# Optimization experiments

Hardware: AMD Instinct MI355X
Metric: run time of the kernel (lower is better)

Reference implementation:

```python
import jax, jax.numpy as jnp
import numpy as np

N_NODES = 50000
N_EDGES = 800000
D_IN, H1, H2, N_CLASSES = 128, 128, 64, 2


def setup_inputs() -> dict:
    key = jax.random.key(0)
    ks = jax.random.split(key, 8)
    x = jax.random.normal(ks[0], (N_NODES, D_IN), dtype=jnp.float32)
    edge_index = jax.random.randint(ks[1], (2, N_EDGES), 0, N_NODES, dtype=jnp.int64)
    s = 1.0 / np.sqrt(D_IN)
    W1 = jax.random.uniform(ks[2], (D_IN, H1), jnp.float32, -s, s)
    b1 = jnp.zeros((H1,), jnp.float32)
    s = 1.0 / np.sqrt(H1)
    W2 = jax.random.uniform(ks[3], (H1, H2), jnp.float32, -s, s)
    b2 = jnp.zeros((H2,), jnp.float32)
    s = 1.0 / np.sqrt(H2)
    Wo = jax.random.uniform(ks[4], (H2, N_CLASSES), jnp.float32, -s, s)
    bo = jax.random.uniform(ks[5], (N_CLASSES,), jnp.float32, -s, s)
    return {"x": x, "edge_index": edge_index, "W1": W1, "b1": b1,
            "W2": W2, "b2": b2, "Wo": Wo, "bo": bo}


def _gcn_conv(x, W, b, src, dst, n_nodes):
    # PyG GCNConv: add self loops, symmetric normalization deg^{-1/2} A deg^{-1/2}
    h = x @ W  # [N, out]
    ones = jnp.ones((src.shape[0],), h.dtype)
    deg = jax.ops.segment_sum(ones, dst, num_segments=n_nodes) + 1.0  # +1 self loop
    dinv = jax.lax.rsqrt(deg)  # deg >= 1 always (self loops)
    coef = dinv[src] * dinv[dst]  # [E]
    msg = h[src] * coef[:, None]  # [E, out] gather
    agg = jax.ops.segment_sum(msg, dst, num_segments=n_nodes)  # scatter-add
    agg = agg + h * (dinv * dinv)[:, None]  # self-loop contribution
    return agg + b


def reference(x, edge_index, W1, b1, W2, b2, Wo, bo):
    src, dst = edge_index[0], edge_index[1]
    n = x.shape[0]
    h = jax.nn.relu(_gcn_conv(x, W1, b1, src, dst, n))
    # dropout p=0.25 is identity in eval mode
    h = jax.nn.relu(_gcn_conv(h, W2, b2, src, dst, n))
    logits = h @ Wo + bo
    return jax.nn.log_softmax(logits, axis=1)
```

## Files before the change

kernel.cpp:

```cpp
#include <hip/hip_runtime.h>
#include <stdint.h>

#define N_NODES 50000
#define N_EDGES 800000
#define CAP 80
#define ZROW N_NODES
#define SCAT_BLOCKS 391
#define GEMM_BLOCKS 782
#define CNT(v) ((v) << 4)

typedef __attribute__((ext_vector_type(8))) short short8;
typedef __attribute__((ext_vector_type(4))) float floatx4;

__device__ __forceinline__ float bflo(uint32_t u) { return __uint_as_float(u << 16); }
__device__ __forceinline__ float bfhi(uint32_t u) { return __uint_as_float(u & 0xffff0000u); }
__device__ __forceinline__ unsigned short f2b(float f) {
    uint32_t u = __float_as_uint(f);
    u += 0x7fffu + ((u >> 16) & 1u);
    return (unsigned short)(u >> 16);
}

__global__ void k_prep(const float* __restrict__ W1, const float* __restrict__ W2,
                       unsigned short* __restrict__ Wt1, unsigned short* __restrict__ Wt2,
                       int* __restrict__ counts) {
    int gid = blockIdx.x * 256 + threadIdx.x;
    if (gid < 16384) {
        int k = gid >> 7, n = gid & 127;
        Wt1[n * 128 + k] = f2b(W1[gid]);
    } else if (gid < 24576) {
        int j = gid - 16384;
        int k = j >> 6, n = j & 63;
        Wt2[n * 128 + k] = f2b(W2[j]);
    } else if (gid < 24576 + 802816) {
        counts[gid - 24576] = 0;
    }
}

__global__ __launch_bounds__(256) void k_scat_gemm1(const int* __restrict__ src,
                                                    const int* __restrict__ dst,
                                                    int* __restrict__ counts,
                                                    int* __restrict__ csr,
                                                    const float* __restrict__ x,
                                                    const unsigned short* __restrict__ Wt1,
                                                    unsigned short* __restrict__ h1s,
                                                    unsigned short* __restrict__ h2s) {
    __shared__ unsigned short At[64 * 136];
    __shared__ unsigned short Bt[128 * 136];
    int t = threadIdx.x;
    if (blockIdx.x < SCAT_BLOCKS) {
        int i = blockIdx.x * 256 + t;
        if (i >= N_EDGES / 8) return;
        const int4* s4 = (const int4*)(src + i * 8);
        const int4* d4 = (const int4*)(dst + i * 8);
        int4 sa = s4[0], sb = s4[1];
        int4 da = d4[0], db = d4[1];
        int r0 = atomicAdd(&counts[CNT(da.x)], 1);
        int r1 = atomicAdd(&counts[CNT(da.y)], 1);
        int r2 = atomicAdd(&counts[CNT(da.z)], 1);
        int r3 = atomicAdd(&counts[CNT(da.w)], 1);
        int r4 = atomicAdd(&counts[CNT(db.x)], 1);
        int r5 = atomicAdd(&counts[CNT(db.y)], 1);
        int r6 = atomicAdd(&counts[CNT(db.z)], 1);
        int r7 = atomicAdd(&counts[CNT(db.w)], 1);
        if (r0 < CAP) csr[da.x * CAP + r0] = sa.x;
        if (r1 < CAP) csr[da.y * CAP + r1] = sa.y;
        if (r2 < CAP) csr[da.z * CAP + r2] = sa.z;
        if (r3 < CAP) csr[da.w * CAP + r3] = sa.w;
        if (r4 < CAP) csr[db.x * CAP + r4] = sb.x;
        if (r5 < CAP) csr[db.y * CAP + r5] = sb.y;
        if (r6 < CAP) csr[db.z * CAP + r6] = sb.z;
        if (r7 < CAP) csr[db.w * CAP + r7] = sb.w;
        return;
    }
    int row0 = (blockIdx.x - SCAT_BLOCKS) * 64;
    for (int i = t; i < 2048; i += 256) {
        int n = i >> 4, kc = (i & 15) * 8;
        *(uint4*)&Bt[n * 136 + kc] = *(const uint4*)(Wt1 + n * 128 + kc);
    }
    for (int i = t; i < 1024; i += 256) {
        int r = i >> 4, kc = (i & 15) * 8;
        int g = row0 + r; if (g >= N_NODES) g = N_NODES - 1;
        const float* p = x + g * 128 + kc;
        float4 a = *(const float4*)p, b = *(const float4*)(p + 4);
        uint4 o;
        o.x = (uint32_t)f2b(a.x) | ((uint32_t)f2b(a.y) << 16);
        o.y = (uint32_t)f2b(a.z) | ((uint32_t)f2b(a.w) << 16);
        o.z = (uint32_t)f2b(b.x) | ((uint32_t)f2b(b.y) << 16);
        o.w = (uint32_t)f2b(b.z) | ((uint32_t)f2b(b.w) << 16);
        *(uint4*)&At[r * 136 + kc] = o;
    }
    __syncthreads();
    int wv = t >> 6, lane = t & 63;
    int m = lane & 15, qd = lane >> 4;
    floatx4 acc[8];
    #pragma unroll
    for (int c = 0; c < 8; c++) acc[c] = (floatx4){0.f, 0.f, 0.f, 0.f};
    const unsigned short* ap = &At[(wv * 16 + m) * 136 + qd * 8];
    const unsigned short* bp = &Bt[m * 136 + qd * 8];
    #pragma unroll
    for (int kk = 0; kk < 4; kk++) {
        short8 af = *(const short8*)(ap + kk * 32);
        #pragma unroll
        for (int c = 0; c < 8; c++) {
            short8 bf = *(const short8*)(bp + c * 16 * 136 + kk * 32);
            acc[c] = __builtin_amdgcn_mfma_f32_16x16x32_bf16(af, bf, acc[c], 0, 0, 0);
        }
    }
    #pragma unroll
    for (int reg = 0; reg < 4; reg++) {
        int g = row0 + wv * 16 + qd * 4 + reg;
        if (g < N_NODES) {
            #pragma unroll
            for (int c = 0; c < 8; c++)
                h1s[g * 128 + c * 16 + m] = f2b(acc[c][reg]);
        } else {
            #pragma unroll
            for (int c = 0; c < 8; c++)
                h1s[g * 128 + c * 16 + m] = 0;
            #pragma unroll
            for (int c = 0; c < 4; c++)
                h2s[g * 64 + c * 16 + m] = 0;
        }
    }
}

__global__ __launch_bounds__(256) void k_agg1g2(const unsigned short* __restrict__ h1s,
                                                const unsigned short* __restrict__ Wt2,
                                                const int* __restrict__ csr,
                                                const int* __restrict__ counts,
                                                const float* __restrict__ b1,
                                                unsigned short* __restrict__ h2s) {
    __shared__ unsigned short Bt[64 * 136];
    __shared__ unsigned short At[16 * 136];
    int t = threadIdx.x;
    for (int i = t; i < 1024; i += 256) {
        int n = i >> 4, kc = (i & 15) * 8;
        *(uint4*)&Bt[n * 136 + kc] = *(const uint4*)(Wt2 + n * 128 + kc);
    }
    int wv = t >> 6, lane = t & 63;
    int q = lane >> 4, l = lane & 15;
    int v0 = blockIdx.x * 16;
    int v = v0 + wv * 4 + q;
    int n = counts[CNT(v)];
    float dv = rsqrtf((float)n + 1.0f);
    int n_eff = min(n, CAP);
    const int* cs = csr + v * CAP;
    int nmax = n_eff;
    nmax = max(nmax, __shfl_xor(nmax, 16));
    nmax = max(nmax, __shfl_xor(nmax, 32));
    float a0, a1, a2, a3, a4, a5, a6, a7;
    {
        uint4 p = *(const uint4*)(h1s + v * 128 + l * 8);
        a0 = dv * bflo(p.x); a1 = dv * bfhi(p.x); a2 = dv * bflo(p.y); a3 = dv * bfhi(p.y);
        a4 = dv * bflo(p.z); a5 = dv * bfhi(p.z); a6 = dv * bflo(p.w); a7 = dv * bfhi(p.w);
    }
    for (int base = 0; base < nmax; base += 16) {
        int idx = base + l;
        int e = (idx < n_eff) ? cs[idx] : ZROW;
        float de = rsqrtf((float)counts[CNT(e)] + 1.0f);
        int mm = nmax - base; if (mm > 16) mm = 16;
        #pragma unroll 4
        for (int i = 0; i < mm; i++) {
            int s = __shfl(e, (q << 4) + i);
            float di = __shfl(de, (q << 4) + i);
            uint4 p = *(const uint4*)(h1s + s * 128 + l * 8);
            a0 = fmaf(di, bflo(p.x), a0); a1 = fmaf(di, bfhi(p.x), a1);
            a2 = fmaf(di, bflo(p.y), a2); a3 = fmaf(di, bfhi(p.y), a3);
            a4 = fmaf(di, bflo(p.z), a4); a5 = fmaf(di, bfhi(p.z), a5);
            a6 = fmaf(di, bflo(p.w), a6); a7 = fmaf(di, bfhi(p.w), a7);
        }
    }
    {
        float4 bL = *(const float4*)(b1 + l * 8);
        float4 bH = *(const float4*)(b1 + l * 8 + 4);
        a0 = fmaxf(fmaf(dv, a0, bL.x), 0.f); a1 = fmaxf(fmaf(dv, a1, bL.y), 0.f);
        a2 = fmaxf(fmaf(dv, a2, bL.z), 0.f); a3 = fmaxf(fmaf(dv, a3, bL.w), 0.f);
        a4 = fmaxf(fmaf(dv, a4, bH.x), 0.f); a5 = fmaxf(fmaf(dv, a5, bH.y), 0.f);
        a6 = fmaxf(fmaf(dv, a6, bH.z), 0.f); a7 = fmaxf(fmaf(dv, a7, bH.w), 0.f);
        uint4 o;
        o.x = (uint32_t)f2b(a0) | ((uint32_t)f2b(a1) << 16);
        o.y = (uint32_t)f2b(a2) | ((uint32_t)f2b(a3) << 16);
        o.z = (uint32_t)f2b(a4) | ((uint32_t)f2b(a5) << 16);
        o.w = (uint32_t)f2b(a6) | ((uint32_t)f2b(a7) << 16);
        *(uint4*)&At[(wv * 4 + q) * 136 + l * 8] = o;
    }
    __syncthreads();
    int m = lane & 15, qd = lane >> 4;
    floatx4 acc = (floatx4){0.f, 0.f, 0.f, 0.f};
    const unsigned short* ap = &At[m * 136 + qd * 8];
    const unsigned short* bp = &Bt[(wv * 16 + m) * 136 + qd * 8];
    #pragma unroll
    for (int kk = 0; kk < 4; kk++) {
        short8 af = *(const short8*)(ap + kk * 32);
        short8 bf = *(const short8*)(bp + kk * 32);
        acc = __builtin_amdgcn_mfma_f32_16x16x32_bf16(af, bf, acc, 0, 0, 0);
    }
    #pragma unroll
    for (int reg = 0; reg < 4; reg++) {
        int g = v0 + qd * 4 + reg;
        float dg = rsqrtf((float)counts[CNT(g)] + 1.0f);
        h2s[g * 64 + wv * 16 + m] = f2b(dg * acc[reg]);
    }
}

__global__ __launch_bounds__(256) void k_agg2(const unsigned short* __restrict__ h2s,
                                              const int* __restrict__ csr,
                                              const int* __restrict__ counts,
                                              const float* __restrict__ b2,
                                              const float* __restrict__ Wo,
                                              const float* __restrict__ bo,
                                              float* __restrict__ out) {
    int wave = (blockIdx.x * 256 + threadIdx.x) >> 6;
    int lane = threadIdx.x & 63;
    int q = lane >> 4, l = lane & 15;
    int h = l >> 3, c = l & 7;
    int v = wave * 4 + q;
    int n = counts[CNT(v)];
    float dv = rsqrtf((float)n + 1.0f);
    int n_eff = min(n, CAP);
    const int* cs = csr + v * CAP;
    int nmax = n_eff;
    nmax = max(nmax, __shfl_xor(nmax, 16));
    nmax = max(nmax, __shfl_xor(nmax, 32));
    float a0 = 0.f, a1 = 0.f, a2 = 0.f, a3 = 0.f, a4 = 0.f, a5 = 0.f, a6 = 0.f, a7 = 0.f;
    if (h == 0) {
        uint4 p = *(const uint4*)(h2s + v * 64 + c * 8);
        a0 = bflo(p.x); a1 = bfhi(p.x); a2 = bflo(p.y); a3 = bfhi(p.y);
        a4 = bflo(p.z); a5 = bfhi(p.z); a6 = bflo(p.w); a7 = bfhi(p.w);
    }
    for (int base = 0; base < nmax; base += 16) {
        int idx = base + l;
        int e = (idx < n_eff) ? cs[idx] : ZROW;
        int mm = nmax - base; if (mm > 16) mm = 16;
        int pairs = (mm + 1) >> 1;
        #pragma unroll 4
        for (int i = 0; i < pairs; i++) {
            int s = __shfl(e, (q << 4) + 2 * i + h);
            uint4 p = *(const uint4*)(h2s + s * 64 + c * 8);
            a0 += bflo(p.x); a1 += bfhi(p.x); a2 += bflo(p.y); a3 += bfhi(p.y);
            a4 += bflo(p.z); a5 += bfhi(p.z); a6 += bflo(p.w); a7 += bfhi(p.w);
        }
    }
    a0 += __shfl_xor(a0, 8); a1 += __shfl_xor(a1, 8);
    a2 += __shfl_xor(a2, 8); a3 += __shfl_xor(a3, 8);
    a4 += __shfl_xor(a4, 8); a5 += __shfl_xor(a5, 8);
    a6 += __shfl_xor(a6, 8); a7 += __shfl_xor(a7, 8);
    float4 bL = *(const float4*)(b2 + c * 8);
    float4 bH = *(const float4*)(b2 + c * 8 + 4);
    a0 = fmaxf(fmaf(dv, a0, bL.x), 0.f); a1 = fmaxf(fmaf(dv, a1, bL.y), 0.f);
    a2 = fmaxf(fmaf(dv, a2, bL.z), 0.f); a3 = fmaxf(fmaf(dv, a3, bL.w), 0.f);
    a4 = fmaxf(fmaf(dv, a4, bH.x), 0.f); a5 = fmaxf(fmaf(dv, a5, bH.y), 0.f);
    a6 = fmaxf(fmaf(dv, a6, bH.z), 0.f); a7 = fmaxf(fmaf(dv, a7, bH.w), 0.f);
    float4 wA = *(const float4*)(Wo + c * 16);
    float4 wB = *(const float4*)(Wo + c * 16 + 4);
    float4 wC = *(const float4*)(Wo + c * 16 + 8);
    float4 wD = *(const float4*)(Wo + c * 16 + 12);
    float l0 = a0 * wA.x + a1 * wA.z + a2 * wB.x + a3 * wB.z
             + a4 * wC.x + a5 * wC.z + a6 * wD.x + a7 * wD.z;
    float l1 = a0 * wA.y + a1 * wA.w + a2 * wB.y + a3 * wB.w
             + a4 * wC.y + a5 * wC.w + a6 * wD.y + a7 * wD.w;
    l0 += __shfl_xor(l0, 1); l1 += __shfl_xor(l1, 1);
    l0 += __shfl_xor(l0, 2); l1 += __shfl_xor(l1, 2);
    l0 += __shfl_xor(l0, 4); l1 += __shfl_xor(l1, 4);
    if (l == 0) {
        float2 bof = *(const float2*)bo;
        l0 += bof.x; l1 += bof.y;
        float m = fmaxf(l0, l1);
        float ls = m + __logf(__expf(l0 - m) + __expf(l1 - m));
        *(float2*)(out + v * 2) = make_float2(l0 - ls, l1 - ls);
    }
}

extern "C" void kernel_launch(void* const* d_in, const int* in_sizes, int n_in,
                              void* d_out, int out_size, void* d_ws, size_t ws_size,
                              hipStream_t stream) {
    const float* x  = (const float*)d_in[0];
    const int* ei   = (const int*)d_in[1];
    const float* W1 = (const float*)d_in[2];
    const float* b1 = (const float*)d_in[3];
    const float* W2 = (const float*)d_in[4];
    const float* b2 = (const float*)d_in[5];
    const float* Wo = (const float*)d_in[6];
    const float* bo = (const float*)d_in[7];
    float* out      = (float*)d_out;
    const int* src = ei;
    const int* dst = ei + N_EDGES;

    char* w = (char*)d_ws;
    int* counts = (int*)(w + 0);
    int* csr    = (int*)(w + 3211264);
    unsigned short* Wt1 = (unsigned short*)(w + 19211264);
    unsigned short* Wt2 = (unsigned short*)(w + 19244032);
    unsigned short* h1s = (unsigned short*)(w + 19260416);
    unsigned short* h2s = (unsigned short*)(w + 32072704);

    k_prep      <<<3232, 256, 0, stream>>>(W1, W2, Wt1, Wt2, counts);
    k_scat_gemm1<<<SCAT_BLOCKS + GEMM_BLOCKS, 256, 0, stream>>>(src, dst, counts, csr,
                                                                x, Wt1, h1s, h2s);
    k_agg1g2    <<<3125, 256, 0, stream>>>(h1s, Wt2, csr, counts, b1, h2s);
    k_agg2      <<<3125, 256, 0, stream>>>(h2s, csr, counts, b2, Wo, bo, out);
}
```

Before: 183.9 us.

## Build CSR via two-level binned counting sort with shared-memory atomics

Replaces the global-atomic per-edge scatter into padded counts with a two-pass binning scheme. A histogram of destination bins (256 nodes each) is built per block, prefix-scanned by a single-block kernel, and edges are scattered into bin-ordered pairs. Each bin is then placed into the CSR using shared-memory atomics, which also yields compact per-node counts. This removes contended global atomics and the large counts zeroing pass. In exchange it adds two extra kernel launches, a serial single-block scan, and an extra pass over the edges.

```diff
diff --git a/kernel.cpp b/kernel.cpp
--- a/kernel.cpp
+++ b/kernel.cpp
@@ -5,9 +5,10 @@
 #define N_EDGES 800000
 #define CAP 80
 #define ZROW N_NODES
-#define SCAT_BLOCKS 391
+#define NBIN 196
+#define NBLK_A 128
+#define EPB 6250
 #define GEMM_BLOCKS 782
-#define CNT(v) ((v) << 4)
 
 typedef __attribute__((ext_vector_type(8))) short short8;
 typedef __attribute__((ext_vector_type(4))) float floatx4;
@@ -20,10 +21,24 @@
     return (unsigned short)(u >> 16);
 }
 
-__global__ void k_prep(const float* __restrict__ W1, const float* __restrict__ W2,
-                       unsigned short* __restrict__ Wt1, unsigned short* __restrict__ Wt2,
-                       int* __restrict__ counts) {
-    int gid = blockIdx.x * 256 + threadIdx.x;
+__global__ __launch_bounds__(256) void k_prep(const float* __restrict__ W1,
+                                              const float* __restrict__ W2,
+                                              unsigned short* __restrict__ Wt1,
+                                              unsigned short* __restrict__ Wt2,
+                                              const int* __restrict__ dst,
+                                              int* __restrict__ mat) {
+    __shared__ int h[NBIN];
+    int t = threadIdx.x, blk = blockIdx.x;
+    if (blk < NBLK_A) {
+        if (t < NBIN) h[t] = 0;
+        __syncthreads();
+        int e0 = blk * EPB;
+        for (int i = t; i < EPB; i += 256) atomicAdd(&h[dst[e0 + i] >> 8], 1);
+        __syncthreads();
+        if (t < NBIN) mat[blk * NBIN + t] = h[t];
+        return;
+    }
+    int gid = (blk - NBLK_A) * 256 + t;
     if (gid < 16384) {
         int k = gid >> 7, n = gid & 127;
         Wt1[n * 128 + k] = f2b(W1[gid]);
@@ -31,48 +46,81 @@
         int j = gid - 16384;
         int k = j >> 6, n = j & 63;
         Wt2[n * 128 + k] = f2b(W2[j]);
-    } else if (gid < 24576 + 802816) {
-        counts[gid - 24576] = 0;
-    }
-}
-
-__global__ __launch_bounds__(256) void k_scat_gemm1(const int* __restrict__ src,
-                                                    const int* __restrict__ dst,
-                                                    int* __restrict__ counts,
-                                                    int* __restrict__ csr,
-                                                    const float* __restrict__ x,
-                                                    const unsigned short* __restrict__ Wt1,
-                                                    unsigned short* __restrict__ h1s,
-                                                    unsigned short* __restrict__ h2s) {
+    }
+}
+
+__global__ __launch_bounds__(256) void k_scan(int* __restrict__ mat,
+                                              int* __restrict__ binStart) {
+    __shared__ int tot[256];
+    int b = threadIdx.x;
+    int base = 0;
+    if (b < NBIN) {
+        #pragma unroll 8
+        for (int k = 0; k < NBLK_A; k++) {
+            int v = mat[k * NBIN + b];
+            mat[k * NBIN + b] = base;
+            base += v;
+        }
+    }
+    tot[b] = (b < NBIN) ? base : 0;
+    __syncthreads();
+    if (b == 0) {
+        int r = 0;
+        for (int i = 0; i < NBIN; i++) { int v = tot[i]; tot[i] = r; r += v; }
+    }
+    __syncthreads();
+    if (b < NBIN) {
+        int bb = tot[b];
+        binStart[b] = bb;
+        #pragma unroll 8
+        for (int k = 0; k < NBLK_A; k++) mat[k * NBIN + b] += bb;
+        if (b == NBIN - 1) binStart[NBIN] = bb + base;
+    }
+}
+
+__global__ __launch_bounds__(256) void k_binscat(const int* __restrict__ src,
+                                                 const int* __restrict__ dst,
+                                                 const int* __restrict__ mat,
+                                                 int2* __restrict__ binned) {
+    __shared__ int cur[NBIN];
+    int t = threadIdx.x, blk = blockIdx.x;
+    if (t < NBIN) cur[t] = mat[blk * NBIN + t];
+    __syncthreads();
+    int e0 = blk * EPB;
+    for (int i = t; i < EPB; i += 256) {
+        int d = dst[e0 + i], s = src[e0 + i];
+        int slot = atomicAdd(&cur[d >> 8], 1);
+        binned[slot] = make_int2(s, d);
+    }
+}
+
+__global__ __launch_bounds__(256) void k_csr_gemm1(const int2* __restrict__ binned,
+                                                   const int* __restrict__ binStart,
+                                                   int* __restrict__ counts,
+                                                   int* __restrict__ csr,
+                                                   const float* __restrict__ x,
+                                                   const unsigned short* __restrict__ Wt1,
+                                                   unsigned short* __restrict__ h1s,
+                                                   unsigned short* __restrict__ h2s) {
     __shared__ unsigned short At[64 * 136];
     __shared__ unsigned short Bt[128 * 136];
+    __shared__ int cnt[256];
     int t = threadIdx.x;
-    if (blockIdx.x < SCAT_BLOCKS) {
-        int i = blockIdx.x * 256 + t;
-        if (i >= N_EDGES / 8) return;
-        const int4* s4 = (const int4*)(src + i * 8);
-        const int4* d4 = (const int4*)(dst + i * 8);
-        int4 sa = s4[0], sb = s4[1];
-        int4 da = d4[0], db = d4[1];
-        int r0 = atomicAdd(&counts[CNT(da.x)], 1);
-        int r1 = atomicAdd(&counts[CNT(da.y)], 1);
-        int r2 = atomicAdd(&counts[CNT(da.z)], 1);
-        int r3 = atomicAdd(&counts[CNT(da.w)], 1);
-        int r4 = atomicAdd(&counts[CNT(db.x)], 1);
-        int r5 = atomicAdd(&counts[CNT(db.y)], 1);
-        int r6 = atomicAdd(&counts[CNT(db.z)], 1);
-        int r7 = atomicAdd(&counts[CNT(db.w)], 1);
-        if (r0 < CAP) csr[da.x * CAP + r0] = sa.x;
-        if (r1 < CAP) csr[da.y * CAP + r1] = sa.y;
-        if (r2 < CAP) csr[da.z * CAP + r2] = sa.z;
-        if (r3 < CAP) csr[da.w * CAP + r3] = sa.w;
-        if (r4 < CAP) csr[db.x * CAP + r4] = sb.x;
-        if (r5 < CAP) csr[db.y * CAP + r5] = sb.y;
-        if (r6 < CAP) csr[db.z * CAP + r6] = sb.z;
-        if (r7 < CAP) csr[db.w * CAP + r7] = sb.w;
+    if (blockIdx.x < NBIN) {
+        cnt[t] = 0;
+        __syncthreads();
+        int b = blockIdx.x;
+        int st = binStart[b], en = binStart[b + 1];
+        for (int i = st + t; i < en; i += 256) {
+            int2 e = binned[i];
+            int r = atomicAdd(&cnt[e.y & 255], 1);
+            if (r < CAP) csr[e.y * CAP + r] = e.x;
+        }
+        __syncthreads();
+        counts[b * 256 + t] = cnt[t];
         return;
     }
-    int row0 = (blockIdx.x - SCAT_BLOCKS) * 64;
+    int row0 = (blockIdx.x - NBIN) * 64;
     for (int i = t; i < 2048; i += 256) {
         int n = i >> 4, kc = (i & 15) * 8;
         *(uint4*)&Bt[n * 136 + kc] = *(const uint4*)(Wt1 + n * 128 + kc);
@@ -141,7 +189,7 @@
     int q = lane >> 4, l = lane & 15;
     int v0 = blockIdx.x * 16;
     int v = v0 + wv * 4 + q;
-    int n = counts[CNT(v)];
+    int n = counts[v];
     float dv = rsqrtf((float)n + 1.0f);
     int n_eff = min(n, CAP);
     const int* cs = csr + v * CAP;
@@ -157,7 +205,7 @@
     for (int base = 0; base < nmax; base += 16) {
         int idx = base + l;
         int e = (idx < n_eff) ? cs[idx] : ZROW;
-        float de = rsqrtf((float)counts[CNT(e)] + 1.0f);
+        float de = rsqrtf((float)counts[e] + 1.0f);
         int mm = nmax - base; if (mm > 16) mm = 16;
         #pragma unroll 4
         for (int i = 0; i < mm; i++) {
@@ -198,7 +246,7 @@
     #pragma unroll
     for (int reg = 0; reg < 4; reg++) {
         int g = v0 + qd * 4 + reg;
-        float dg = rsqrtf((float)counts[CNT(g)] + 1.0f);
+        float dg = rsqrtf((float)counts[g] + 1.0f);
         h2s[g * 64 + wv * 16 + m] = f2b(dg * acc[reg]);
     }
 }
@@ -215,7 +263,7 @@
     int q = lane >> 4, l = lane & 15;
     int h = l >> 3, c = l & 7;
     int v = wave * 4 + q;
-    int n = counts[CNT(v)];
+    int n = counts[v];
     float dv = rsqrtf((float)n + 1.0f);
     int n_eff = min(n, CAP);
     const int* cs = csr + v * CAP;
@@ -288,15 +336,20 @@
 
     char* w = (char*)d_ws;
     int* counts = (int*)(w + 0);
-    int* csr    = (int*)(w + 3211264);
-    unsigned short* Wt1 = (unsigned short*)(w + 19211264);
-    unsigned short* Wt2 = (unsigned short*)(w + 19244032);
-    unsigned short* h1s = (unsigned short*)(w + 19260416);
-    unsigned short* h2s = (unsigned short*)(w + 32072704);
-
-    k_prep      <<<3232, 256, 0, stream>>>(W1, W2, Wt1, Wt2, counts);
-    k_scat_gemm1<<<SCAT_BLOCKS + GEMM_BLOCKS, 256, 0, stream>>>(src, dst, counts, csr,
-                                                                x, Wt1, h1s, h2s);
-    k_agg1g2    <<<3125, 256, 0, stream>>>(h1s, Wt2, csr, counts, b1, h2s);
-    k_agg2      <<<3125, 256, 0, stream>>>(h2s, csr, counts, b2, Wo, bo, out);
-}
+    int* csr    = (int*)(w + 200704);
+    unsigned short* Wt1 = (unsigned short*)(w + 16200704);
+    unsigned short* Wt2 = (unsigned short*)(w + 16233472);
+    unsigned short* h1s = (unsigned short*)(w + 16249856);
+    unsigned short* h2s = (unsigned short*)(w + 29062144);
+    int2* binned = (int2*)(w + 35468288);
+    int* mat     = (int*)(w + 41868288);
+    int* binStart= (int*)(w + 41968640);
+
+    k_prep     <<<224, 256, 0, stream>>>(W1, W2, Wt1, Wt2, dst, mat);
+    k_scan     <<<1, 256, 0, stream>>>(mat, binStart);
+    k_binscat  <<<NBLK_A, 256, 0, stream>>>(src, dst, mat, binned);
+    k_csr_gemm1<<<NBIN + GEMM_BLOCKS, 256, 0, stream>>>(binned, binStart, counts, csr,
+                                                        x, Wt1, h1s, h2s);
+    k_agg1g2   <<<3125, 256, 0, stream>>>(h1s, Wt2, csr, counts, b1, h2s);
+    k_agg2     <<<3125, 256, 0, stream>>>(h2s, csr, counts, b2, Wo, bo, out);
+}
```

Result: no change. 185.7 us (+1.0%).

## Build CSR via per-block node-range filtering with LDS atomics instead of global atomics

Applied to the files above, without the earlier changes.

Replaces global atomic scatter into padded count slots with 98 blocks that each scan the whole dst array and bucket edges for a 512-node range using shared-memory atomics. This removes the large counts zeroing pass in the prep kernel and makes the counts array compact. In exchange, every filter block rereads all destination indices, multiplying read traffic, and the filter blocks run long serial loops.

```diff
diff --git a/kernel.cpp b/kernel.cpp
--- a/kernel.cpp
+++ b/kernel.cpp
@@ -5,9 +5,8 @@
 #define N_EDGES 800000
 #define CAP 80
 #define ZROW N_NODES
-#define SCAT_BLOCKS 391
+#define NFILT 98
 #define GEMM_BLOCKS 782
-#define CNT(v) ((v) << 4)
 
 typedef __attribute__((ext_vector_type(8))) short short8;
 typedef __attribute__((ext_vector_type(4))) float floatx4;
@@ -20,9 +19,10 @@
     return (unsigned short)(u >> 16);
 }
 
-__global__ void k_prep(const float* __restrict__ W1, const float* __restrict__ W2,
-                       unsigned short* __restrict__ Wt1, unsigned short* __restrict__ Wt2,
-                       int* __restrict__ counts) {
+__global__ __launch_bounds__(256) void k_prep(const float* __restrict__ W1,
+                                              const float* __restrict__ W2,
+                                              unsigned short* __restrict__ Wt1,
+                                              unsigned short* __restrict__ Wt2) {
     int gid = blockIdx.x * 256 + threadIdx.x;
     if (gid < 16384) {
         int k = gid >> 7, n = gid & 127;
@@ -31,48 +31,43 @@
         int j = gid - 16384;
         int k = j >> 6, n = j & 63;
         Wt2[n * 128 + k] = f2b(W2[j]);
-    } else if (gid < 24576 + 802816) {
-        counts[gid - 24576] = 0;
-    }
-}
-
-__global__ __launch_bounds__(256) void k_scat_gemm1(const int* __restrict__ src,
-                                                    const int* __restrict__ dst,
-                                                    int* __restrict__ counts,
-                                                    int* __restrict__ csr,
-                                                    const float* __restrict__ x,
-                                                    const unsigned short* __restrict__ Wt1,
-                                                    unsigned short* __restrict__ h1s,
-                                                    unsigned short* __restrict__ h2s) {
+    }
+}
+
+__global__ __launch_bounds__(256) void k_csr_gemm1(const int* __restrict__ src,
+                                                   const int* __restrict__ dst,
+                                                   int* __restrict__ counts,
+                                                   int* __restrict__ csr,
+                                                   const float* __restrict__ x,
+                                                   const unsigned short* __restrict__ Wt1,
+                                                   unsigned short* __restrict__ h1s,
+                                                   unsigned short* __restrict__ h2s) {
     __shared__ unsigned short At[64 * 136];
     __shared__ unsigned short Bt[128 * 136];
     int t = threadIdx.x;
-    if (blockIdx.x < SCAT_BLOCKS) {
-        int i = blockIdx.x * 256 + t;
-        if (i >= N_EDGES / 8) return;
-        const int4* s4 = (const int4*)(src + i * 8);
-        const int4* d4 = (const int4*)(dst + i * 8);
-        int4 sa = s4[0], sb = s4[1];
-        int4 da = d4[0], db = d4[1];
-        int r0 = atomicAdd(&counts[CNT(da.x)], 1);
-        int r1 = atomicAdd(&counts[CNT(da.y)], 1);
-        int r2 = atomicAdd(&counts[CNT(da.z)], 1);
-        int r3 = atomicAdd(&counts[CNT(da.w)], 1);
-        int r4 = atomicAdd(&counts[CNT(db.x)], 1);
-        int r5 = atomicAdd(&counts[CNT(db.y)], 1);
-        int r6 = atomicAdd(&counts[CNT(db.z)], 1);
-        int r7 = atomicAdd(&counts[CNT(db.w)], 1);
-        if (r0 < CAP) csr[da.x * CAP + r0] = sa.x;
-        if (r1 < CAP) csr[da.y * CAP + r1] = sa.y;
-        if (r2 < CAP) csr[da.z * CAP + r2] = sa.z;
-        if (r3 < CAP) csr[da.w * CAP + r3] = sa.w;
-        if (r4 < CAP) csr[db.x * CAP + r4] = sb.x;
-        if (r5 < CAP) csr[db.y * CAP + r5] = sb.y;
-        if (r6 < CAP) csr[db.z * CAP + r6] = sb.z;
-        if (r7 < CAP) csr[db.w * CAP + r7] = sb.w;
+    if (blockIdx.x < NFILT) {
+        int* cnt = (int*)At;
+        cnt[t] = 0; cnt[t + 256] = 0;
+        __syncthreads();
+        int node0 = blockIdx.x << 9;
+        const int4* d4 = (const int4*)dst;
+        for (int j = t; j < 200000; j += 256) {
+            int4 dv = d4[j];
+            unsigned o0 = (unsigned)(dv.x - node0);
+            unsigned o1 = (unsigned)(dv.y - node0);
+            unsigned o2 = (unsigned)(dv.z - node0);
+            unsigned o3 = (unsigned)(dv.w - node0);
+            if (o0 < 512u) { int r = atomicAdd(&cnt[o0], 1); if (r < CAP) csr[dv.x * CAP + r] = src[j * 4 + 0]; }
+            if (o1 < 512u) { int r = atomicAdd(&cnt[o1], 1); if (r < CAP) csr[dv.y * CAP + r] = src[j * 4 + 1]; }
+            if (o2 < 512u) { int r = atomicAdd(&cnt[o2], 1); if (r < CAP) csr[dv.z * CAP + r] = src[j * 4 + 2]; }
+            if (o3 < 512u) { int r = atomicAdd(&cnt[o3], 1); if (r < CAP) csr[dv.w * CAP + r] = src[j * 4 + 3]; }
+        }
+        __syncthreads();
+        counts[node0 + t] = cnt[t];
+        counts[node0 + 256 + t] = cnt[t + 256];
         return;
     }
-    int row0 = (blockIdx.x - SCAT_BLOCKS) * 64;
+    int row0 = (blockIdx.x - NFILT) * 64;
     for (int i = t; i < 2048; i += 256) {
         int n = i >> 4, kc = (i & 15) * 8;
         *(uint4*)&Bt[n * 136 + kc] = *(const uint4*)(Wt1 + n * 128 + kc);
@@ -141,7 +136,7 @@
     int q = lane >> 4, l = lane & 15;
     int v0 = blockIdx.x * 16;
     int v = v0 + wv * 4 + q;
-    int n = counts[CNT(v)];
+    int n = counts[v];
     float dv = rsqrtf((float)n + 1.0f);
     int n_eff = min(n, CAP);
     const int* cs = csr + v * CAP;
@@ -157,7 +152,7 @@
     for (int base = 0; base < nmax; base += 16) {
         int idx = base + l;
         int e = (idx < n_eff) ? cs[idx] : ZROW;
-        float de = rsqrtf((float)counts[CNT(e)] + 1.0f);
+        float de = rsqrtf((float)counts[e] + 1.0f);
         int mm = nmax - base; if (mm > 16) mm = 16;
         #pragma unroll 4
         for (int i = 0; i < mm; i++) {
@@ -198,7 +193,7 @@
     #pragma unroll
     for (int reg = 0; reg < 4; reg++) {
         int g = v0 + qd * 4 + reg;
-        float dg = rsqrtf((float)counts[CNT(g)] + 1.0f);
+        float dg = rsqrtf((float)counts[g] + 1.0f);
         h2s[g * 64 + wv * 16 + m] = f2b(dg * acc[reg]);
     }
 }
@@ -215,7 +210,7 @@
     int q = lane >> 4, l = lane & 15;
     int h = l >> 3, c = l & 7;
     int v = wave * 4 + q;
-    int n = counts[CNT(v)];
+    int n = counts[v];
     float dv = rsqrtf((float)n + 1.0f);
     int n_eff = min(n, CAP);
     const int* cs = csr + v * CAP;
@@ -288,15 +283,15 @@
 
     char* w = (char*)d_ws;
     int* counts = (int*)(w + 0);
-    int* csr    = (int*)(w + 3211264);
-    unsigned short* Wt1 = (unsigned short*)(w + 19211264);
-    unsigned short* Wt2 = (unsigned short*)(w + 19244032);
-    unsigned short* h1s = (unsigned short*)(w + 19260416);
-    unsigned short* h2s = (unsigned short*)(w + 32072704);
-
-    k_prep      <<<3232, 256, 0, stream>>>(W1, W2, Wt1, Wt2, counts);
-    k_scat_gemm1<<<SCAT_BLOCKS + GEMM_BLOCKS, 256, 0, stream>>>(src, dst, counts, csr,
-                                                                x, Wt1, h1s, h2s);
-    k_agg1g2    <<<3125, 256, 0, stream>>>(h1s, Wt2, csr, counts, b1, h2s);
-    k_agg2      <<<3125, 256, 0, stream>>>(h2s, csr, counts, b2, Wo, bo, out);
-}
+    int* csr    = (int*)(w + 200704);
+    unsigned short* Wt1 = (unsigned short*)(w + 16200704);
+    unsigned short* Wt2 = (unsigned short*)(w + 16233472);
+    unsigned short* h1s = (unsigned short*)(w + 16249856);
+    unsigned short* h2s = (unsigned short*)(w + 29062144);
+
+    k_prep     <<<96, 256, 0, stream>>>(W1, W2, Wt1, Wt2);
+    k_csr_gemm1<<<NFILT + GEMM_BLOCKS, 256, 0, stream>>>(src, dst, counts, csr,
+                                                         x, Wt1, h1s, h2s);
+    k_agg1g2   <<<3125, 256, 0, stream>>>(h1s, Wt2, csr, counts, b1, h2s);
+    k_agg2     <<<3125, 256, 0, stream>>>(h2s, csr, counts, b2, Wo, bo, out);
+}
```

New measurement: 652.2 us. 255% more time.
